# Kernel optimization log

Measured on AMD Instinct MI355X. Metric: run time of the kernel, lower is better.

Reference implementation:

```python
import jax, jax.numpy as jnp
import numpy as np

B, N, DIM, H, DH = 8, 1024, 768, 12, 64  # batch, seq, d_model, heads, dim_head
INNER = H * DH


def setup_inputs() -> dict:
    key = jax.random.key(0)
    ks = jax.random.split(key, 6)
    s = 1.0 / np.sqrt(DIM)
    return {
        "x": jax.random.normal(ks[0], (B, N, DIM), dtype=jnp.float32),
        "Wq": jax.random.normal(ks[1], (DIM, INNER), dtype=jnp.float32) * s,
        "Wkv": jax.random.normal(ks[2], (DIM, 2 * INNER), dtype=jnp.float32) * s,
        "mix_pre": jax.random.normal(ks[3], (H, H), dtype=jnp.float32) * (1.0 / H),
        "mix_post": jax.random.normal(ks[4], (H, H), dtype=jnp.float32) * (1.0 / H),
        "Wo": jax.random.normal(ks[5], (INNER, DIM), dtype=jnp.float32) * s,
        "bo": jnp.zeros((DIM,), dtype=jnp.float32),
    }


def reference(x, Wq, Wkv, mix_pre, mix_post, Wo, bo):
    scale = DH ** -0.5
    q = x @ Wq                                   # [B,N,INNER]
    kv = x @ Wkv                                 # [B,N,2*INNER]
    k, v = jnp.split(kv, 2, axis=-1)
    split_heads = lambda t: t.reshape(B, N, H, DH).transpose(0, 2, 1, 3)  # [B,H,N,DH]
    q, k, v = split_heads(q), split_heads(k), split_heads(v)
    dots = jnp.einsum('bhid,bhjd->bhij', q, k) * scale
    dots = jnp.einsum('bhij,hg->bgij', dots, mix_pre)      # talking-heads pre-softmax
    attn = jax.nn.softmax(dots, axis=-1)
    attn = jnp.einsum('bhij,hg->bgij', attn, mix_post)     # talking-heads post-softmax
    o = jnp.einsum('bhij,bhjd->bhid', attn, v)             # [B,H,N,DH]
    o = o.transpose(0, 2, 1, 3).reshape(B, N, INNER)
    return o @ Wo + bo
```

## Files before the change

### kernel.cpp

```cpp
#include <hip/hip_runtime.h>
#include <cstdint>
#include <cstddef>

typedef unsigned short u16;
typedef unsigned int u32;

typedef __bf16 bf16x8 __attribute__((ext_vector_type(8)));
typedef float f32x4 __attribute__((ext_vector_type(4)));
typedef u32 u32x4 __attribute__((ext_vector_type(4)));
typedef u32 u32x2 __attribute__((ext_vector_type(2)));

#if defined(__has_builtin)
#if __has_builtin(__builtin_amdgcn_global_load_lds)
#define USE_GLL 1
#endif
#endif

typedef const __attribute__((address_space(1))) u32 gas_u32;
typedef __attribute__((address_space(3))) u32 las_u32;

__device__ inline float bf2f(u16 u) {
    union { u32 i; float f; } c; c.i = ((u32)u) << 16; return c.f;
}
__device__ inline u16 f2bf(float f) {
    union { float f; u32 i; } c; c.f = f;
    u32 u = c.i;
    return (u16)((u + 0x7fffu + ((u >> 16) & 1u)) >> 16);
}
__device__ inline f32x4 mfma16(u32x4 a, u32x4 b, f32x4 c) {
    return __builtin_amdgcn_mfma_f32_16x16x32_bf16(
        __builtin_bit_cast(bf16x8, a), __builtin_bit_cast(bf16x8, b), c, 0, 0, 0);
}
__device__ inline u32x4 cvt8(const float* p) {
    f32x4 a = *(const f32x4*)p, b = *(const f32x4*)(p + 4);
    u32x4 v;
    v[0] = (u32)f2bf(a[0]) | ((u32)f2bf(a[1]) << 16);
    v[1] = (u32)f2bf(a[2]) | ((u32)f2bf(a[3]) << 16);
    v[2] = (u32)f2bf(b[0]) | ((u32)f2bf(b[1]) << 16);
    v[3] = (u32)f2bf(b[2]) | ((u32)f2bf(b[3]) << 16);
    return v;
}

__global__ __launch_bounds__(64) void k_detect(const u16* __restrict__ x, u32* __restrict__ flag)
{
    const int lane = threadIdx.x;
    int cnt = 0;
#pragma unroll
    for (int i = 0; i < 4; i++) {
        u32 e = (x[lane * 4 + i] >> 7) & 0xFF;
        cnt += (e >= 115 && e <= 133) ? 1 : 0;
    }
#pragma unroll
    for (int off = 1; off < 64; off <<= 1) cnt += __shfl_xor(cnt, off);
    if (lane == 0) *flag = (cnt >= 192) ? 1u : 0u;
}

__global__ __launch_bounds__(256) void k_convert_x(
    const void* __restrict__ X, u16* __restrict__ xb, const u32* __restrict__ flag)
{
    const bool isb = (*flag != 0);
    const size_t i = ((size_t)blockIdx.x * 256 + threadIdx.x) * 8;
    if (isb) *(u32x4*)(xb + i) = *(const u32x4*)((const u16*)X + i);
    else     *(u32x4*)(xb + i) = cvt8((const float*)X + i);
}

__global__ __launch_bounds__(256) void k_transpose_w(
    const void* __restrict__ Wq, const void* __restrict__ Wkv, const void* __restrict__ Wo,
    u16* __restrict__ WT, u16* __restrict__ WoT, const u32* __restrict__ flag)
{
    const bool isb = (*flag != 0);
    __shared__ __align__(16) u16 t[64][72];
    const int z = blockIdx.z;
    const void* src; u16* dst; int C;
    if (z == 0)      { src = Wq;  dst = WT;             C = 768;  }
    else if (z == 1) { src = Wkv; dst = WT + 768 * 768; C = 1536; }
    else             { src = Wo;  dst = WoT;            C = 768;  }
    const int c0 = blockIdx.y * 64;
    if (c0 >= C) return;
    const int k0 = blockIdx.x * 64;
    const int tid = threadIdx.x;
    const int r = tid >> 3, cc = (tid & 7) * 8;
    if (isb) {
        const u16* s = (const u16*)src;
        for (int rr = r; rr < 64; rr += 32)
            *(u32x4*)&t[rr][cc] = *(const u32x4*)(s + (size_t)(k0 + rr) * C + c0 + cc);
    } else {
        const float* s = (const float*)src;
        for (int rr = r; rr < 64; rr += 32)
            *(u32x4*)&t[rr][cc] = cvt8(s + (size_t)(k0 + rr) * C + c0 + cc);
    }
    __syncthreads();
    const int kk = (tid & 7) * 8;
    for (int ccc = tid >> 3; ccc < 64; ccc += 32) {
        __align__(16) u16 tmp[8];
#pragma unroll
        for (int s = 0; s < 8; s++) tmp[s] = t[kk + s][ccc];
        *(u32x4*)(dst + (size_t)(c0 + ccc) * 768 + k0 + kk) = *(u32x4*)tmp;
    }
}

__global__ __launch_bounds__(256) void k_transpose_v(
    const u16* __restrict__ v, u16* __restrict__ vt)
{
    __shared__ __align__(16) u16 t[64][72];
    const int bh = blockIdx.z;
    const int t0 = blockIdx.x * 64;
    const int tid = threadIdx.x;
    const int r = tid >> 3, cc = (tid & 7) * 8;
    for (int rr = r; rr < 64; rr += 32)
        *(u32x4*)&t[rr][cc] = *(const u32x4*)(v + ((size_t)bh * 1024 + t0 + rr) * 64 + cc);
    __syncthreads();
    const int kk = (tid & 7) * 8;
    for (int ccc = tid >> 3; ccc < 64; ccc += 32) {
        __align__(16) u16 tmp[8];
#pragma unroll
        for (int s = 0; s < 8; s++) tmp[s] = t[kk + s][ccc];
        *(u32x4*)(vt + ((size_t)bh * 64 + ccc) * 1024 + t0 + kk) = *(u32x4*)tmp;
    }
}

__device__ inline void stage_tile(const u16* __restrict__ gA, const u16* __restrict__ gB,
                                  u16* As, u16* Bs, int w, int lane)
{
    const int sr = lane >> 2, sc = (lane & 3) * 8;
#pragma unroll
    for (int i = 0; i < 2; i++) {
        const int rA = w * 16 + i * 64;
        const u16* ga = gA + (size_t)(rA + sr) * 768 + sc;
        const u16* gb = gB + (size_t)(rA + sr) * 768 + sc;
#ifdef USE_GLL
        __builtin_amdgcn_global_load_lds((gas_u32*)ga, (las_u32*)&As[rA * 32], 16, 0, 0);
        __builtin_amdgcn_global_load_lds((gas_u32*)gb, (las_u32*)&Bs[rA * 32], 16, 0, 0);
#else
        *(u32x4*)&As[(rA + sr) * 32 + sc] = *(const u32x4*)ga;
        *(u32x4*)&Bs[(rA + sr) * 32 + sc] = *(const u32x4*)gb;
#endif
    }
}

__global__ __launch_bounds__(256) void k_gemm_qkv(
    const u16* __restrict__ Xb, const u16* __restrict__ WT,
    u16* __restrict__ qb, u16* __restrict__ kb, u16* __restrict__ vb)
{
    __shared__ __align__(16) u16 As[128 * 32];
    __shared__ __align__(16) u16 Bs[128 * 32];
    const int tid = threadIdx.x;
    const int w = tid >> 6, lane = tid & 63, quad = lane >> 4, l15 = lane & 15;
    const int wr = w >> 1, wc = w & 1;
    const int m0 = blockIdx.y * 128, c0 = blockIdx.x * 128;
    f32x4 acc[4][4];
#pragma unroll
    for (int i = 0; i < 4; i++)
#pragma unroll
        for (int j = 0; j < 4; j++) acc[i][j] = (f32x4){0.f, 0.f, 0.f, 0.f};

    for (int k0 = 0; k0 < 768; k0 += 32) {
        __syncthreads();
        stage_tile(Xb + (size_t)m0 * 768 + k0, WT + (size_t)c0 * 768 + k0, As, Bs, w, lane);
        __syncthreads();
        u32x4 af[4], bfv[4];
#pragma unroll
        for (int mi = 0; mi < 4; mi++)
            af[mi] = *(const u32x4*)&As[(wr * 64 + mi * 16 + l15) * 32 + quad * 8];
#pragma unroll
        for (int ni = 0; ni < 4; ni++)
            bfv[ni] = *(const u32x4*)&Bs[(wc * 64 + ni * 16 + l15) * 32 + quad * 8];
#pragma unroll
        for (int mi = 0; mi < 4; mi++)
#pragma unroll
            for (int ni = 0; ni < 4; ni++)
                acc[mi][ni] = mfma16(af[mi], bfv[ni], acc[mi][ni]);
    }
#pragma unroll
    for (int mi = 0; mi < 4; mi++)
#pragma unroll
        for (int ni = 0; ni < 4; ni++) {
            const int c = c0 + wc * 64 + ni * 16 + l15;
            const int sector = c / 768, hc = c % 768;
            const int h = hc >> 6, d = hc & 63;
            u16* dst = sector == 0 ? qb : (sector == 1 ? kb : vb);
#pragma unroll
            for (int r = 0; r < 4; r++) {
                const int tok = m0 + wr * 64 + mi * 16 + quad * 4 + r;
                const int b = tok >> 10, n = tok & 1023;
                dst[(((size_t)b * 12 + h) * 1024 + n) * 64 + d] = f2bf(acc[mi][ni][r]);
            }
        }
}

__global__ __launch_bounds__(256) void k_gemm_out(
    const u16* __restrict__ O, const u16* __restrict__ WoT, const void* __restrict__ bo,
    float* __restrict__ out, const u32* __restrict__ flag)
{
    const bool isb = (*flag != 0);
    __shared__ __align__(16) u16 As[128 * 32];
    __shared__ __align__(16) u16 Bs[128 * 32];
    const int tid = threadIdx.x;
    const int w = tid >> 6, lane = tid & 63, quad = lane >> 4, l15 = lane & 15;
    const int wr = w >> 1, wc = w & 1;
    const int m0 = blockIdx.y * 128, c0 = blockIdx.x * 128;
    f32x4 acc[4][4];
#pragma unroll
    for (int i = 0; i < 4; i++)
#pragma unroll
        for (int j = 0; j < 4; j++) acc[i][j] = (f32x4){0.f, 0.f, 0.f, 0.f};

    for (int k0 = 0; k0 < 768; k0 += 32) {
        __syncthreads();
        stage_tile(O + (size_t)m0 * 768 + k0, WoT + (size_t)c0 * 768 + k0, As, Bs, w, lane);
        __syncthreads();
        u32x4 af[4], bfv[4];
#pragma unroll
        for (int mi = 0; mi < 4; mi++)
            af[mi] = *(const u32x4*)&As[(wr * 64 + mi * 16 + l15) * 32 + quad * 8];
#pragma unroll
        for (int ni = 0; ni < 4; ni++)
            bfv[ni] = *(const u32x4*)&Bs[(wc * 64 + ni * 16 + l15) * 32 + quad * 8];
#pragma unroll
        for (int mi = 0; mi < 4; mi++)
#pragma unroll
            for (int ni = 0; ni < 4; ni++)
                acc[mi][ni] = mfma16(af[mi], bfv[ni], acc[mi][ni]);
    }
#pragma unroll
    for (int mi = 0; mi < 4; mi++)
#pragma unroll
        for (int ni = 0; ni < 4; ni++) {
            const int c = c0 + wc * 64 + ni * 16 + l15;
            const float biasv = isb ? bf2f(((const u16*)bo)[c]) : ((const float*)bo)[c];
#pragma unroll
            for (int r = 0; r < 4; r++) {
                const int tok = m0 + wr * 64 + mi * 16 + quad * 4 + r;
                out[(size_t)tok * 768 + c] = acc[mi][ni][r] + biasv;
            }
        }
}

__global__ __launch_bounds__(768) void k_attn(
    const u16* __restrict__ qb, const u16* __restrict__ kb, const u16* __restrict__ vt,
    const void* __restrict__ mixpre, const void* __restrict__ mixpost,
    u16* __restrict__ ob, u16* __restrict__ E, const u32* __restrict__ flag, int tiles)
{
    __shared__ __align__(16) u16 LDSU[18432];
    __shared__ float invlT[256];
    u16* SP   = LDSU;
    u32* SP32 = (u32*)LDSU;
    u16* Abuf = LDSU;
    float* red = (float*)LDSU;

    const bool isb = (*flag != 0);
    const int tid = threadIdx.x;
    const int w = tid >> 6, lane = tid & 63, quad = lane >> 4, l15 = lane & 15;
    const int bid = blockIdx.x;
    const int b = bid & 7;
    const int nq = gridDim.x >> 3;
    u16* Ewg = E + (size_t)bid * (16384 * 12);

    u32x4 apre = (u32x4){0, 0, 0, 0};
    float mpostF[8];
#pragma unroll
    for (int j = 0; j < 8; j++) {
        const int h = quad * 8 + j;
        mpostF[j] = 0.f;
        if (quad < 2 && l15 < 12 && h < 12) {
            mpostF[j] = isb ? bf2f(((const u16*)mixpost)[h * 12 + l15])
                            : ((const float*)mixpost)[h * 12 + l15];
            u16 v1 = isb ? ((const u16*)mixpre)[h * 12 + l15]
                         : f2bf(((const float*)mixpre)[h * 12 + l15]);
            apre[j >> 1] |= ((u32)v1) << ((j & 1) * 16);
        }
    }

    const u16* kh = kb + ((size_t)b * 12 + w) * 1024 * 64;
    const u16* vh = vt + ((size_t)b * 12 + w) * 64 * 1024;

    for (int tt = 0; tt < tiles; tt++) {
        const int qx = (bid >> 3) + tt * nq;
        const int i0 = qx * 16;

        for (int n = tid; n < 1024; n += 768) { SP32[n * 9 + 6] = 0; SP32[n * 9 + 7] = 0; }

        const u16* qh = qb + (((size_t)b * 12 + w) * 1024 + i0) * 64;
        u32x4 aq[2];
#pragma unroll
        for (int kc = 0; kc < 2; kc++)
            aq[kc] = *(const u32x4*)(qh + l15 * 64 + kc * 32 + quad * 8);

        f32x4 part[6];
#pragma unroll
        for (int t = 0; t < 6; t++) part[t] = (f32x4){0.f, 0.f, 0.f, 0.f};

        for (int jt = 0; jt < 16; jt++) {
            const int j0 = jt * 64;
            f32x4 sc[4];
#pragma unroll
            for (int nt = 0; nt < 4; nt++) {
                f32x4 a = (f32x4){0.f, 0.f, 0.f, 0.f};
#pragma unroll
                for (int kc = 0; kc < 2; kc++) {
                    u32x4 bfr = *(const u32x4*)(kh + (size_t)(j0 + nt * 16 + l15) * 64 + kc * 32 + quad * 8);
                    a = mfma16(aq[kc], bfr, a);
                }
                sc[nt] = a;
            }
            __syncthreads();
#pragma unroll
            for (int nt = 0; nt < 4; nt++)
#pragma unroll
                for (int r = 0; r < 4; r++)
                    SP[((quad * 4 + r) * 64 + nt * 16 + l15) * 18 + w] = f2bf(sc[nt][r] * 0.125f);
            __syncthreads();
#pragma unroll
            for (int t = 0; t < 6; t++) {
                const int s = w + 12 * t;
                if (s < 64) {
                    const int row = s * 16 + l15;
                    u32x4 bfr = (u32x4){0, 0, 0, 0};
                    if (quad < 2) {
                        const u32* p = SP32 + row * 9 + quad * 4;
                        bfr[0] = p[0]; bfr[1] = p[1]; bfr[2] = p[2]; bfr[3] = p[3];
                    }
                    f32x4 d = mfma16(apre, bfr, (f32x4){0.f, 0.f, 0.f, 0.f});
                    const float e0 = __expf(d[0]), e1 = __expf(d[1]);
                    const float e2 = __expf(d[2]), e3 = __expf(d[3]);
                    part[t][0] += e0; part[t][1] += e1;
                    part[t][2] += e2; part[t][3] += e3;
                    if (quad < 3) {
                        u32x2 pk;
                        pk[0] = (u32)f2bf(e0) | ((u32)f2bf(e1) << 16);
                        pk[1] = (u32)f2bf(e2) | ((u32)f2bf(e3) << 16);
                        *(u32x2*)(Ewg + ((size_t)jt * 1024 + row) * 12 + quad * 4) = pk;
                    }
                }
            }
        }
        __syncthreads();
#pragma unroll
        for (int t = 0; t < 6; t++) {
            const int s = w + 12 * t;
            if (s < 64) {
#pragma unroll
                for (int r = 0; r < 4; r++) {
                    float v = part[t][r];
#pragma unroll
                    for (int off = 1; off < 16; off <<= 1) v += __shfl_xor(v, off);
                    if (l15 == 0) red[(((s >> 2) * 16) + quad * 4 + r) * 4 + (s & 3)] = v;
                }
            }
        }
        __syncthreads();
        if (tid < 256) {
            const int h = tid & 15;
            float v = 0.f;
            if (h < 12) {
                const float* q = &red[tid * 4];
                v = 1.f / (q[0] + q[1] + q[2] + q[3]);
            }
            invlT[tid] = v;
        }
        __syncthreads();

        u32x4 Afr[6];
#pragma unroll
        for (int t = 0; t < 6; t++) {
            const int s = w + 12 * t;
            Afr[t] = (u32x4){0, 0, 0, 0};
            if (s < 64 && quad < 2) {
                const int i = s >> 2;
#pragma unroll
                for (int j = 0; j < 8; j++) {
                    const u16 v = f2bf(mpostF[j] * invlT[i * 16 + quad * 8 + j]);
                    Afr[t][j >> 1] |= ((u32)v) << ((j & 1) * 16);
                }
            }
        }

        f32x4 oacc[4];
#pragma unroll
        for (int nt = 0; nt < 4; nt++) oacc[nt] = (f32x4){0.f, 0.f, 0.f, 0.f};

        for (int jt = 0; jt < 16; jt++) {
            const int j0 = jt * 64;
#pragma unroll
            for (int t = 0; t < 6; t++) {
                const int s = w + 12 * t;
                if (s < 64) {
                    const int row = s * 16 + l15, i = s >> 2, jq = s & 3;
                    u32x4 ef = (u32x4){0, 0, 0, 0};
                    if (quad < 2) {
                        const u16* ep = Ewg + ((size_t)jt * 1024 + row) * 12 + quad * 8;
                        u32x2 lo = *(const u32x2*)ep;
                        u32x2 hi = *(const u32x2*)(ep + 4);
                        ef[0] = lo[0]; ef[1] = lo[1]; ef[2] = hi[0]; ef[3] = hi[1];
                    }
                    f32x4 am = mfma16(Afr[t], ef, (f32x4){0.f, 0.f, 0.f, 0.f});
#pragma unroll
                    for (int r = 0; r < 4; r++) {
                        const int g2 = quad * 4 + r;
                        if (g2 < 12)
                            Abuf[g2 * 1160 + i * 72 + jq * 16 + l15] = f2bf(am[r]);
                    }
                }
            }
            __syncthreads();
#pragma unroll
            for (int kc = 0; kc < 2; kc++) {
                u32x4 af = *(const u32x4*)&Abuf[w * 1160 + l15 * 72 + kc * 32 + quad * 8];
#pragma unroll
                for (int nt = 0; nt < 4; nt++) {
                    u32x4 vf = *(const u32x4*)(vh + (size_t)(nt * 16 + l15) * 1024 + j0 + kc * 32 + quad * 8);
                    oacc[nt] = mfma16(af, vf, oacc[nt]);
                }
            }
            __syncthreads();
        }
#pragma unroll
        for (int nt = 0; nt < 4; nt++)
#pragma unroll
            for (int r = 0; r < 4; r++)
                ob[((size_t)b * 1024 + i0 + quad * 4 + r) * 768 + w * 64 + nt * 16 + l15] =
                    f2bf(oacc[nt][r]);
    }
}

extern "C" void kernel_launch(void* const* d_in, const int* in_sizes, int n_in,
                              void* d_out, int out_size, void* d_ws, size_t ws_size,
                              hipStream_t stream)
{
    float* out = (float*)d_out;

    u32* flag = (u32*)d_ws;
    u16* WoT  = (u16*)d_ws + 128;
    u16* qb   = WoT + 768 * 768;
    u16* kb   = qb  + 6291456;
    u16* vtb  = kb  + 6291456;
    u16* obuf = vtb + 6291456;
    u16* vb   = obuf;
    u16* ez   = obuf + 6291456;
    u16* WT   = ez;
    u16* xb   = ez + 2304 * 768;
    u16* E    = ez;

    const size_t base   = 256 + 2ull * (768 * 768 + 4ull * 6291456);
    const size_t eslot  = 16384ull * 12 * 2;
    const size_t need1  = base + 512ull * eslot + 64;
    const size_t need2  = base + 256ull * eslot + 64;

    k_detect     <<<dim3(1), 64,  0, stream>>>((const u16*)d_in[0], flag);
    k_transpose_w<<<dim3(12, 24, 3), 256, 0, stream>>>(d_in[1], d_in[2], d_in[5], WT, WoT, flag);
    k_convert_x  <<<dim3(3072),      256, 0, stream>>>(d_in[0], xb, flag);
    k_gemm_qkv   <<<dim3(18, 64),    256, 0, stream>>>(xb, WT, qb, kb, vb);
    k_transpose_v<<<dim3(16, 1, 96), 256, 0, stream>>>(vb, vtb);
    if (ws_size >= need1)
        k_attn   <<<dim3(512), 768, 0, stream>>>(qb, kb, vtb, d_in[3], d_in[4], obuf, E, flag, 1);
    else
        k_attn   <<<dim3(256), 768, 0, stream>>>(qb, kb, vtb, d_in[3], d_in[4], obuf, E, flag, 2);
    k_gemm_out   <<<dim3(6, 64),     256, 0, stream>>>(obuf, WoT, d_in[6], out, flag);
}
```

Measured before the change: 466.3 us.

## Fuse V transpose into QKV GEMM epilogue and double attention PV tile width

The QKV GEMM epilogue now writes V directly in transposed [b,h,d,n] layout, so the separate transpose kernel and its extra round trip through global memory are removed. The attention kernel's PV loop now processes 128 keys per step instead of 64, with a larger LDS buffer, which halves the number of block-wide barriers. The transposed V stores are strided per lane and less coalesced, and the larger LDS footprint may lower occupancy.

```diff
diff --git a/kernel.cpp b/kernel.cpp
--- a/kernel.cpp
+++ b/kernel.cpp
@@ -99,26 +99,6 @@
     }
 }
 
-__global__ __launch_bounds__(256) void k_transpose_v(
-    const u16* __restrict__ v, u16* __restrict__ vt)
-{
-    __shared__ __align__(16) u16 t[64][72];
-    const int bh = blockIdx.z;
-    const int t0 = blockIdx.x * 64;
-    const int tid = threadIdx.x;
-    const int r = tid >> 3, cc = (tid & 7) * 8;
-    for (int rr = r; rr < 64; rr += 32)
-        *(u32x4*)&t[rr][cc] = *(const u32x4*)(v + ((size_t)bh * 1024 + t0 + rr) * 64 + cc);
-    __syncthreads();
-    const int kk = (tid & 7) * 8;
-    for (int ccc = tid >> 3; ccc < 64; ccc += 32) {
-        __align__(16) u16 tmp[8];
-#pragma unroll
-        for (int s = 0; s < 8; s++) tmp[s] = t[kk + s][ccc];
-        *(u32x4*)(vt + ((size_t)bh * 64 + ccc) * 1024 + t0 + kk) = *(u32x4*)tmp;
-    }
-}
-
 __device__ inline void stage_tile(const u16* __restrict__ gA, const u16* __restrict__ gB,
                                   u16* As, u16* Bs, int w, int lane)
 {
@@ -140,7 +120,7 @@
 
 __global__ __launch_bounds__(256) void k_gemm_qkv(
     const u16* __restrict__ Xb, const u16* __restrict__ WT,
-    u16* __restrict__ qb, u16* __restrict__ kb, u16* __restrict__ vb)
+    u16* __restrict__ qb, u16* __restrict__ kb, u16* __restrict__ vt)
 {
     __shared__ __align__(16) u16 As[128 * 32];
     __shared__ __align__(16) u16 Bs[128 * 32];
@@ -171,21 +151,37 @@
             for (int ni = 0; ni < 4; ni++)
                 acc[mi][ni] = mfma16(af[mi], bfv[ni], acc[mi][ni]);
     }
-#pragma unroll
-    for (int mi = 0; mi < 4; mi++)
-#pragma unroll
-        for (int ni = 0; ni < 4; ni++) {
-            const int c = c0 + wc * 64 + ni * 16 + l15;
-            const int sector = c / 768, hc = c % 768;
-            const int h = hc >> 6, d = hc & 63;
-            u16* dst = sector == 0 ? qb : (sector == 1 ? kb : vb);
-#pragma unroll
-            for (int r = 0; r < 4; r++) {
-                const int tok = m0 + wr * 64 + mi * 16 + quad * 4 + r;
-                const int b = tok >> 10, n = tok & 1023;
-                dst[(((size_t)b * 12 + h) * 1024 + n) * 64 + d] = f2bf(acc[mi][ni][r]);
-            }
-        }
+    if (c0 >= 1536) {
+#pragma unroll
+        for (int mi = 0; mi < 4; mi++)
+#pragma unroll
+            for (int ni = 0; ni < 4; ni++) {
+                const int hc = c0 - 1536 + wc * 64 + ni * 16 + l15;
+                const int h = hc >> 6, d = hc & 63;
+#pragma unroll
+                for (int r = 0; r < 4; r++) {
+                    const int tok = m0 + wr * 64 + mi * 16 + quad * 4 + r;
+                    const int b = tok >> 10, n = tok & 1023;
+                    vt[(((size_t)b * 12 + h) * 64 + d) * 1024 + n] = f2bf(acc[mi][ni][r]);
+                }
+            }
+    } else {
+#pragma unroll
+        for (int mi = 0; mi < 4; mi++)
+#pragma unroll
+            for (int ni = 0; ni < 4; ni++) {
+                const int c = c0 + wc * 64 + ni * 16 + l15;
+                const int sector = c / 768, hc = c % 768;
+                const int h = hc >> 6, d = hc & 63;
+                u16* dst = sector == 0 ? qb : kb;
+#pragma unroll
+                for (int r = 0; r < 4; r++) {
+                    const int tok = m0 + wr * 64 + mi * 16 + quad * 4 + r;
+                    const int b = tok >> 10, n = tok & 1023;
+                    dst[(((size_t)b * 12 + h) * 1024 + n) * 64 + d] = f2bf(acc[mi][ni][r]);
+                }
+            }
+    }
 }
 
 __global__ __launch_bounds__(256) void k_gemm_out(
@@ -241,7 +237,7 @@
     const void* __restrict__ mixpre, const void* __restrict__ mixpost,
     u16* __restrict__ ob, u16* __restrict__ E, const u32* __restrict__ flag, int tiles)
 {
-    __shared__ __align__(16) u16 LDSU[18432];
+    __shared__ __align__(16) u16 LDSU[27648];
     __shared__ float invlT[256];
     u16* SP   = LDSU;
     u32* SP32 = (u32*)LDSU;
@@ -379,33 +375,37 @@
 #pragma unroll
         for (int nt = 0; nt < 4; nt++) oacc[nt] = (f32x4){0.f, 0.f, 0.f, 0.f};
 
-        for (int jt = 0; jt < 16; jt++) {
-            const int j0 = jt * 64;
-#pragma unroll
-            for (int t = 0; t < 6; t++) {
-                const int s = w + 12 * t;
-                if (s < 64) {
-                    const int row = s * 16 + l15, i = s >> 2, jq = s & 3;
-                    u32x4 ef = (u32x4){0, 0, 0, 0};
-                    if (quad < 2) {
-                        const u16* ep = Ewg + ((size_t)jt * 1024 + row) * 12 + quad * 8;
-                        u32x2 lo = *(const u32x2*)ep;
-                        u32x2 hi = *(const u32x2*)(ep + 4);
-                        ef[0] = lo[0]; ef[1] = lo[1]; ef[2] = hi[0]; ef[3] = hi[1];
+        for (int jt2 = 0; jt2 < 8; jt2++) {
+            const int j0 = jt2 * 128;
+#pragma unroll
+            for (int jh = 0; jh < 2; jh++) {
+                const int jt = jt2 * 2 + jh;
+#pragma unroll
+                for (int t = 0; t < 6; t++) {
+                    const int s = w + 12 * t;
+                    if (s < 64) {
+                        const int row = s * 16 + l15, i = s >> 2, jq = s & 3;
+                        u32x4 ef = (u32x4){0, 0, 0, 0};
+                        if (quad < 2) {
+                            const u16* ep = Ewg + ((size_t)jt * 1024 + row) * 12 + quad * 8;
+                            u32x2 lo = *(const u32x2*)ep;
+                            u32x2 hi = *(const u32x2*)(ep + 4);
+                            ef[0] = lo[0]; ef[1] = lo[1]; ef[2] = hi[0]; ef[3] = hi[1];
+                        }
+                        f32x4 am = mfma16(Afr[t], ef, (f32x4){0.f, 0.f, 0.f, 0.f});
+#pragma unroll
+                        for (int r = 0; r < 4; r++) {
+                            const int g2 = quad * 4 + r;
+                            if (g2 < 12)
+                                Abuf[g2 * 2208 + i * 136 + jh * 64 + jq * 16 + l15] = f2bf(am[r]);
+                        }
                     }
-                    f32x4 am = mfma16(Afr[t], ef, (f32x4){0.f, 0.f, 0.f, 0.f});
-#pragma unroll
-                    for (int r = 0; r < 4; r++) {
-                        const int g2 = quad * 4 + r;
-                        if (g2 < 12)
-                            Abuf[g2 * 1160 + i * 72 + jq * 16 + l15] = f2bf(am[r]);
-                    }
                 }
             }
             __syncthreads();
 #pragma unroll
-            for (int kc = 0; kc < 2; kc++) {
-                u32x4 af = *(const u32x4*)&Abuf[w * 1160 + l15 * 72 + kc * 32 + quad * 8];
+            for (int kc = 0; kc < 4; kc++) {
+                u32x4 af = *(const u32x4*)&Abuf[w * 2208 + l15 * 136 + kc * 32 + quad * 8];
 #pragma unroll
                 for (int nt = 0; nt < 4; nt++) {
                     u32x4 vf = *(const u32x4*)(vh + (size_t)(nt * 16 + l15) * 1024 + j0 + kc * 32 + quad * 8);
@@ -435,7 +435,6 @@
     u16* kb   = qb  + 6291456;
     u16* vtb  = kb  + 6291456;
     u16* obuf = vtb + 6291456;
-    u16* vb   = obuf;
     u16* ez   = obuf + 6291456;
     u16* WT   = ez;
     u16* xb   = ez + 2304 * 768;
@@ -444,13 +443,11 @@
     const size_t base   = 256 + 2ull * (768 * 768 + 4ull * 6291456);
     const size_t eslot  = 16384ull * 12 * 2;
     const size_t need1  = base + 512ull * eslot + 64;
-    const size_t need2  = base + 256ull * eslot + 64;
 
     k_detect     <<<dim3(1), 64,  0, stream>>>((const u16*)d_in[0], flag);
     k_transpose_w<<<dim3(12, 24, 3), 256, 0, stream>>>(d_in[1], d_in[2], d_in[5], WT, WoT, flag);
     k_convert_x  <<<dim3(3072),      256, 0, stream>>>(d_in[0], xb, flag);
-    k_gemm_qkv   <<<dim3(18, 64),    256, 0, stream>>>(xb, WT, qb, kb, vb);
-    k_transpose_v<<<dim3(16, 1, 96), 256, 0, stream>>>(vb, vtb);
+    k_gemm_qkv   <<<dim3(18, 64),    256, 0, stream>>>(xb, WT, qb, kb, vtb);
     if (ws_size >= need1)
         k_attn   <<<dim3(512), 768, 0, stream>>>(qb, kb, vtb, d_in[3], d_in[4], obuf, E, flag, 1);
     else
```

Result: slower. 503.5 us (+8.0%).
